# Kernel optimization log

Measured on AMD Instinct MI355X. Metric: run time of the kernel, lower is better.

The kernel has to match this reference:

```python
import jax, jax.numpy as jnp
import numpy as np

C = 256
C8 = C // 8
B, H, W = 4, 64, 64


def setup_inputs() -> dict:
    key = jax.random.key(0)
    ks = jax.random.split(key, 10)
    s = lambda fan_in: 1.0 / np.sqrt(fan_in)
    return {
        "x": jax.random.normal(ks[0], (B, C, H, W), dtype=jnp.float32),
        "conv_w": jax.random.normal(ks[1], (C8, C), dtype=jnp.float32) * s(C),
        "conv_b": jax.random.normal(ks[2], (C8,), dtype=jnp.float32) * 0.01,
        "q_w": jax.random.normal(ks[3], (C8, C8), dtype=jnp.float32) * s(C8),
        "q_b": jax.random.normal(ks[4], (C8,), dtype=jnp.float32) * 0.01,
        "k_w": jax.random.normal(ks[5], (C8, C8), dtype=jnp.float32) * s(C8),
        "k_b": jax.random.normal(ks[6], (C8,), dtype=jnp.float32) * 0.01,
        "v_w": jax.random.normal(ks[7], (C, C8), dtype=jnp.float32) * s(C8),
        "v_b": jax.random.normal(ks[8], (C,), dtype=jnp.float32) * 0.01,
        "gamma": jax.random.normal(ks[9], (1,), dtype=jnp.float32) * 0.1,
    }


def reference(x, conv_w, conv_b, q_w, q_b, k_w, k_b, v_w, v_b, gamma):
    b, c, h, w = x.shape
    hw = h * w
    # 1x1 convs are channel-mixing matmuls over flattened spatial dims
    xf = x.reshape(b, c, hw)                                   # [B, C, HW]
    proj = jnp.einsum('dc,bcn->bdn', conv_w, xf) + conv_b[None, :, None]   # [B, C8, HW]
    q = jnp.einsum('ed,bdn->bne', q_w, proj) + q_b[None, None, :]          # [B, HW, C8]
    k = jnp.einsum('ed,bdn->ben', k_w, proj) + k_b[None, :, None]          # [B, C8, HW]
    v = jnp.einsum('cd,bdn->bcn', v_w, proj) + v_b[None, :, None]          # [B, C, HW]
    attn = jax.nn.softmax(jnp.einsum('bne,bem->bnm', q, k), axis=-1)       # [B, HW, HW]
    out = jnp.einsum('bcm,bnm->bcn', v, attn)                              # [B, C, HW]
    out = out.reshape(b, c, h, w)
    return gamma[0] * out + x
```

## Files before the change

### kernel.cpp

```cpp
#include <hip/hip_runtime.h>
#include <hip/hip_bf16.h>
#include <stdint.h>

#define B_   4
#define C_   256
#define C8_  32
#define HW_  4096
#define ROWS_ 320
#define MS_  4
#define L2E  1.4426950408889634f

typedef __attribute__((ext_vector_type(8)))  short  short8;
typedef __attribute__((ext_vector_type(8)))  ushort us8;
typedef __attribute__((ext_vector_type(16))) float  f32x16;

#define WT_OFF    0
#define BALL_OFF  (256*320*4)
#define Q_OFF     (BALL_OFF + 1280)
#define KT_OFF    (Q_OFF  + B_*HW_*C8_*2)
#define V_OFF     (KT_OFF + B_*HW_*C8_*2)
#define PACC_OFF  (V_OFF  + B_*C_*HW_*2)
#define LPART_OFF (PACC_OFF + (size_t)MS_*B_*C_*HW_*2)

__device__ __forceinline__ ushort f2bf(float f) {
    union { float f; uint32_t u; } v; v.f = f;
    uint32_t u = v.u;
    uint32_t r = u + 0x7fffu + ((u >> 16) & 1u);
    return (ushort)(r >> 16);
}
__device__ __forceinline__ uint32_t pktr(float lo, float hi) {
    union { float f; uint32_t u; } a, b; a.f = lo; b.f = hi;
    return __builtin_amdgcn_perm(b.u, a.u, 0x07060302u);
}
__device__ __forceinline__ float fexp2(float s) {
    float y = fmaf(s, 8388608.0f, 1064992506.0f);
    y = fmaxf(y, 0.0f);
    union { int i; float f; } c; c.i = (int)y;
    return c.f;
}

__global__ __launch_bounds__(256) void k_setup(
    const float* __restrict__ conv_w, const float* __restrict__ conv_b,
    const float* __restrict__ q_w, const float* __restrict__ q_b,
    const float* __restrict__ k_w, const float* __restrict__ k_b,
    const float* __restrict__ v_w, const float* __restrict__ v_b,
    ushort* __restrict__ wbf, float* __restrict__ ball)
{
    int r = blockIdx.x;
    int c = threadIdx.x;
    const float* wrow;
    float bias;
    if (r < 32)       { wrow = q_w + r*32;      bias = q_b[r];      }
    else if (r < 64)  { wrow = k_w + (r-32)*32; bias = k_b[r-32];   }
    else              { wrow = v_w + (r-64)*32; bias = v_b[r-64];   }
    float acc = 0.f;
    #pragma unroll
    for (int d = 0; d < 32; ++d) acc += wrow[d] * conv_w[d*C_ + c];
    float scale = (r < 32) ? L2E : 1.0f;
    wbf[r*C_ + c] = f2bf(acc * scale);
    if (c == 0) {
        float bb = bias;
        #pragma unroll
        for (int d = 0; d < 32; ++d) bb += wrow[d] * conv_b[d];
        ball[r] = bb * scale;
    }
}

__global__ __launch_bounds__(320) void k_qkv(
    const float* __restrict__ x, const ushort* __restrict__ wbf,
    const float* __restrict__ ball,
    ushort* __restrict__ qg, ushort* __restrict__ ktg, ushort* __restrict__ vg)
{
    int blk = blockIdx.x;
    int b  = blk >> 7;
    int n0 = (blk & 127) * 32;
    int t = threadIdx.x;
    int w = t >> 6, lane = t & 63;
    int l31 = lane & 31, h = lane >> 5;

    f32x16 acc[2];
    acc[0] = (f32x16)(0.f);
    acc[1] = (f32x16)(0.f);

    const float* xb = x + (size_t)b*C_*HW_ + n0 + l31;
    const ushort* wr0 = wbf + (size_t)(w*64 + l31)*C_ + h*8;
    const ushort* wr1 = wr0 + 32*C_;

    #pragma unroll 2
    for (int kc = 0; kc < 16; ++kc) {
        int k0 = kc*16;
        short8 a0 = *(const short8*)(wr0 + k0);
        short8 a1 = *(const short8*)(wr1 + k0);
        const float* xc = xb + (size_t)(k0 + h*8)*HW_;
        union { uint32_t d[4]; short8 s8; } bf;
        #pragma unroll
        for (int j2 = 0; j2 < 4; ++j2) {
            float f0 = xc[(size_t)(2*j2    )*HW_];
            float f1 = xc[(size_t)(2*j2 + 1)*HW_];
            bf.d[j2] = pktr(f0, f1);
        }
        acc[0] = __builtin_amdgcn_mfma_f32_32x32x16_bf16(a0, bf.s8, acc[0], 0, 0, 0);
        acc[1] = __builtin_amdgcn_mfma_f32_32x32x16_bf16(a1, bf.s8, acc[1], 0, 0, 0);
    }

    int n = n0 + l31;
    #pragma unroll
    for (int mi = 0; mi < 2; ++mi) {
        int rowb = w*64 + mi*32;
        if (rowb == 0) {
            #pragma unroll
            for (int g = 0; g < 4; ++g) {
                int r0 = g*8 + 4*h;
                ushort4 pk;
                pk.x = f2bf(acc[mi][g*4+0] + ball[r0+0]);
                pk.y = f2bf(acc[mi][g*4+1] + ball[r0+1]);
                pk.z = f2bf(acc[mi][g*4+2] + ball[r0+2]);
                pk.w = f2bf(acc[mi][g*4+3] + ball[r0+3]);
                *(ushort4*)(qg + ((size_t)b*HW_ + n)*C8_ + r0) = pk;
            }
        } else if (rowb == 32) {
            #pragma unroll
            for (int g = 0; g < 4; ++g) {
                int e0 = g*8 + 4*h;
                ushort4 pk;
                pk.x = f2bf(acc[mi][g*4+0] + ball[32+e0+0]);
                pk.y = f2bf(acc[mi][g*4+1] + ball[32+e0+1]);
                pk.z = f2bf(acc[mi][g*4+2] + ball[32+e0+2]);
                pk.w = f2bf(acc[mi][g*4+3] + ball[32+e0+3]);
                *(ushort4*)(ktg + ((size_t)b*HW_ + n)*C8_ + e0) = pk;
            }
        } else {
            #pragma unroll
            for (int r = 0; r < 16; ++r) {
                int roff = (r & 3) + 8*(r >> 2) + 4*h;
                int c = rowb - 64 + roff;
                vg[((size_t)b*C_ + c)*HW_ + n] = f2bf(acc[mi][r] + ball[rowb + roff]);
            }
        }
    }
}

__global__ __launch_bounds__(256, 2) void k_attn(
    const ushort* __restrict__ qg, const ushort* __restrict__ ktg,
    const ushort* __restrict__ vg,
    ushort* __restrict__ pacc, float* __restrict__ lpart)
{
    __shared__ ushort v_lds[2][16*512];
    __shared__ ushort kt_lds[2][4*512];

    int blk = blockIdx.x;
    int ms = blk & 3;
    int cs = (blk >> 2) & 1;
    int qb = (blk >> 3) & 15;
    int b  = blk >> 7;
    int t = threadIdx.x;
    int w = t >> 6, lane = t & 63;
    int l31 = lane & 31, h = lane >> 5;
    int qbase = qb*256 + w*64;
    int mbase = ms*1024;

    const ushort* kb_p = ktg + (size_t)b*HW_*C8_;
    const ushort* vb_p = vg  + (size_t)b*C_*HW_ + (size_t)cs*128*HW_;

    short8 qf[2][2];
    #pragma unroll
    for (int qfr = 0; qfr < 2; ++qfr)
        #pragma unroll
        for (int ks = 0; ks < 2; ++ks)
            qf[qfr][ks] = *(const short8*)(qg + ((size_t)b*HW_ + qbase + qfr*32 + l31)*C8_
                                           + ks*16 + h*8);

    f32x16 acc[2][4];
    #pragma unroll
    for (int i = 0; i < 2; ++i)
        #pragma unroll
        for (int j = 0; j < 4; ++j)
            acc[i][j] = (f32x16)(0.f);
    float lsum[2] = {0.f, 0.f};

    #define STAGE(buf, m0)                                                          \
    {                                                                               \
        _Pragma("unroll")                                                           \
        for (int ks = 0; ks < 4; ++ks) {                                            \
            const ushort* src = vb_p + (size_t)(w*32 + l31)*HW_                     \
                                + (m0) + ks*16 + h*8;                               \
            __builtin_amdgcn_global_load_lds(                                       \
                (const __attribute__((address_space(1))) uint32_t*)src,             \
                (__attribute__((address_space(3))) uint32_t*)&v_lds[buf][(w*4+ks)*512], \
                16, 0, 0);                                                          \
        }                                                                           \
        {                                                                           \
            int kb = w >> 1, ks = w & 1;                                            \
            const ushort* src = kb_p + (size_t)((m0) + kb*32 + l31)*C8_             \
                                + ks*16 + h*8;                                      \
            __builtin_amdgcn_global_load_lds(                                       \
                (const __attribute__((address_space(1))) uint32_t*)src,             \
                (__attribute__((address_space(3))) uint32_t*)&kt_lds[buf][w*512],   \
                16, 0, 0);                                                          \
        }                                                                           \
    }

    STAGE(0, mbase)
    __syncthreads();

    int buf = 0;
    for (int it = 0; it < 16; ++it) {
        if (it + 1 < 16) STAGE(buf ^ 1, mbase + (it+1)*64)

        short8 ktf[2][2];
        #pragma unroll
        for (int kb = 0; kb < 2; ++kb)
            #pragma unroll
            for (int ks = 0; ks < 2; ++ks)
                ktf[kb][ks] = *(const short8*)(&kt_lds[buf][(kb*2+ks)*512 + lane*8]);

        uint32_t up[4][8];
        #pragma unroll
        for (int qfr = 0; qfr < 2; ++qfr) {
            #pragma unroll
            for (int kb = 0; kb < 2; ++kb) {
                f32x16 s = (f32x16)(0.f);
                s = __builtin_amdgcn_mfma_f32_32x32x16_bf16(ktf[kb][0], qf[qfr][0], s, 0, 0, 0);
                s = __builtin_amdgcn_mfma_f32_32x32x16_bf16(ktf[kb][1], qf[qfr][1], s, 0, 0, 0);
                float e[16];
                #pragma unroll
                for (int r = 0; r < 16; ++r) e[r] = fexp2(s[r]);
                float t0 = 0.f, t1 = 0.f;
                #pragma unroll
                for (int r = 0; r < 8; ++r) { t0 += e[2*r]; t1 += e[2*r+1]; }
                lsum[qfr] += t0 + t1;
                #pragma unroll
                for (int i = 0; i < 8; ++i)
                    up[qfr*2+kb][i] = pktr(e[2*i], e[2*i+1]);
            }
        }

        short8 pf[2][4];
        #pragma unroll
        for (int qfr = 0; qfr < 2; ++qfr) {
            #pragma unroll
            for (int kb = 0; kb < 2; ++kb) {
                uint32_t* u = up[qfr*2+kb];
                uint32_t bpA = (uint32_t)__shfl_xor((int)(h ? u[0] : u[2]), 32);
                uint32_t bpB = (uint32_t)__shfl_xor((int)(h ? u[1] : u[3]), 32);
                uint32_t bpC = (uint32_t)__shfl_xor((int)(h ? u[4] : u[6]), 32);
                uint32_t bpD = (uint32_t)__shfl_xor((int)(h ? u[5] : u[7]), 32);
                union { uint32_t d[4]; short8 s8; } fe, fo;
                fe.d[0] = h ? bpA : u[0];  fe.d[1] = h ? bpB : u[1];
                fe.d[2] = h ? u[2] : bpA;  fe.d[3] = h ? u[3] : bpB;
                fo.d[0] = h ? bpC : u[4];  fo.d[1] = h ? bpD : u[5];
                fo.d[2] = h ? u[6] : bpC;  fo.d[3] = h ? u[7] : bpD;
                pf[qfr][kb*2 + 0] = fe.s8;
                pf[qfr][kb*2 + 1] = fo.s8;
            }
        }

        #pragma unroll
        for (int ks = 0; ks < 4; ++ks) {
            #pragma unroll
            for (int cfr = 0; cfr < 4; ++cfr) {
                short8 vf = *(const short8*)(&v_lds[buf][(cfr*4+ks)*512 + lane*8]);
                acc[0][cfr] = __builtin_amdgcn_mfma_f32_32x32x16_bf16(vf, pf[0][ks], acc[0][cfr], 0, 0, 0);
                acc[1][cfr] = __builtin_amdgcn_mfma_f32_32x32x16_bf16(vf, pf[1][ks], acc[1][cfr], 0, 0, 0);
            }
        }
        __syncthreads();
        buf ^= 1;
    }

    #pragma unroll
    for (int qfr = 0; qfr < 2; ++qfr) {
        union { float f; int i; } cv; cv.f = lsum[qfr];
        cv.i = __shfl_xor(cv.i, 32);
        lsum[qfr] += cv.f;
    }
    if (cs == 0 && h == 0) {
        #pragma unroll
        for (int qfr = 0; qfr < 2; ++qfr)
            lpart[(size_t)(ms*B_ + b)*HW_ + qbase + qfr*32 + l31] = lsum[qfr];
    }

    int blkl = ((ms*B_ + b)*16 + qb)*2 + cs;
    #pragma unroll
    for (int qfr = 0; qfr < 2; ++qfr) {
        #pragma unroll
        for (int cfr = 0; cfr < 4; ++cfr) {
            union { uint32_t d[8]; us8 hlf[2]; } pk;
            #pragma unroll
            for (int i = 0; i < 8; ++i)
                pk.d[i] = pktr(acc[qfr][cfr][2*i], acc[qfr][cfr][2*i+1]);
            ushort* dst = pacc + ((size_t)(blkl*32 + (w*2 + qfr)*4 + cfr) << 10);
            *(us8*)(dst + lane*8)       = pk.hlf[0];
            *(us8*)(dst + 512 + lane*8) = pk.hlf[1];
        }
    }
    #undef STAGE
}

__global__ __launch_bounds__(256) void k_comb(
    const ushort* __restrict__ pacc, const float* __restrict__ lpart,
    const float* __restrict__ x, const float* __restrict__ gamma_p,
    float* __restrict__ out)
{
    int gid = blockIdx.x * 256 + threadIdx.x;
    int l31 = gid & 31;
    int h   = (gid >> 5) & 1;
    int cfr = (gid >> 6) & 3;
    int qfr = (gid >> 8) & 1;
    int w   = (gid >> 9) & 3;
    int cs  = (gid >> 11) & 1;
    int qb  = (gid >> 12) & 15;
    int b   = (gid >> 16) & 3;

    int q = qb*256 + w*64 + qfr*32 + l31;
    int frag = (w*2 + qfr)*4 + cfr;
    int lane = h*32 + l31;

    float sum[16];
    #pragma unroll
    for (int k = 0; k < 16; ++k) sum[k] = 0.f;
    float lt = 0.f;

    #pragma unroll
    for (int ms = 0; ms < MS_; ++ms) {
        int blkl = ((ms*B_ + b)*16 + qb)*2 + cs;
        const ushort* pp = pacc + ((size_t)(blkl*32 + frag) << 10) + lane*8;
        us8 a0 = *(const us8*)pp;
        us8 a1 = *(const us8*)(pp + 512);
        #pragma unroll
        for (int k = 0; k < 8; ++k) {
            union { uint32_t u; float f; } cv;
            cv.u = ((uint32_t)a0[k]) << 16;  sum[k]   += cv.f;
            cv.u = ((uint32_t)a1[k]) << 16;  sum[k+8] += cv.f;
        }
        lt += lpart[(size_t)(ms*B_ + b)*HW_ + q];
    }

    float g = gamma_p[0];
    float rl = g / lt;
    const float* xb = x + (size_t)b*C_*HW_ + q;
    float* ob = out + (size_t)b*C_*HW_ + q;
    #pragma unroll
    for (int k = 0; k < 16; ++k) {
        int c = cs*128 + cfr*32 + (k & 3) + 8*(k >> 2) + 4*h;
        size_t idx = (size_t)c*HW_;
        ob[idx] = sum[k]*rl + xb[idx];
    }
}

extern "C" void kernel_launch(void* const* d_in, const int* in_sizes, int n_in,
                              void* d_out, int out_size, void* d_ws, size_t ws_size,
                              hipStream_t stream)
{
    const float* x      = (const float*)d_in[0];
    const float* conv_w = (const float*)d_in[1];
    const float* conv_b = (const float*)d_in[2];
    const float* q_w    = (const float*)d_in[3];
    const float* q_b    = (const float*)d_in[4];
    const float* k_w    = (const float*)d_in[5];
    const float* k_b    = (const float*)d_in[6];
    const float* v_w    = (const float*)d_in[7];
    const float* v_b    = (const float*)d_in[8];
    const float* gamma  = (const float*)d_in[9];
    float* out = (float*)d_out;

    char* ws = (char*)d_ws;
    ushort* wbf   = (ushort*)(ws + WT_OFF);
    float*  ball  = (float*)(ws + BALL_OFF);
    ushort* qg    = (ushort*)(ws + Q_OFF);
    ushort* ktg   = (ushort*)(ws + KT_OFF);
    ushort* vg    = (ushort*)(ws + V_OFF);
    ushort* pacc  = (ushort*)(ws + PACC_OFF);
    float*  lpart = (float*)(ws + LPART_OFF);

    k_setup<<<ROWS_, 256, 0, stream>>>(conv_w, conv_b, q_w, q_b, k_w, k_b,
                                       v_w, v_b, wbf, ball);
    k_qkv<<<B_*128, 320, 0, stream>>>(x, wbf, ball, qg, ktg, vg);
    k_attn<<<512, 256, 0, stream>>>(qg, ktg, vg, pacc, lpart);
    k_comb<<<(B_*HW_*C_/16)/256, 256, 0, stream>>>(pacc, lpart, x, gamma, out);
}
```

Baseline: 179.0 us.

## Store Q/K/V and weights in MFMA fragment-native layout; double KV tile per stage

The setup and QKV kernels now write the fused weights, Q, K^T and V directly in a pre-swizzled fragment layout, with each 64-lane fragment contiguous in 512 elements. The attention kernel can then issue fully contiguous global-to-LDS loads and 16-byte per-lane reads instead of strided row gathers. The attention inner loop also stages 128 key positions per iteration instead of 64, which halves the number of barriers and pipeline steps. In exchange it doubles the LDS footprint, which may limit occupancy under launch_bounds(256,2). The V store in the QKV kernel is now scattered across fragment offsets.

```diff
diff --git a/kernel.cpp b/kernel.cpp
--- a/kernel.cpp
+++ b/kernel.cpp
@@ -57,7 +57,9 @@
     #pragma unroll
     for (int d = 0; d < 32; ++d) acc += wrow[d] * conv_w[d*C_ + c];
     float scale = (r < 32) ? L2E : 1.0f;
-    wbf[r*C_ + c] = f2bf(acc * scale);
+    int lanew = (r & 31) + 32*((c >> 3) & 1);
+    int fidx  = (c >> 4)*10 + (r >> 5);
+    wbf[fidx*512 + lanew*8 + (c & 7)] = f2bf(acc * scale);
     if (c == 0) {
         float bb = bias;
         #pragma unroll
@@ -83,14 +85,12 @@
     acc[1] = (f32x16)(0.f);
 
     const float* xb = x + (size_t)b*C_*HW_ + n0 + l31;
-    const ushort* wr0 = wbf + (size_t)(w*64 + l31)*C_ + h*8;
-    const ushort* wr1 = wr0 + 32*C_;
 
     #pragma unroll 2
     for (int kc = 0; kc < 16; ++kc) {
         int k0 = kc*16;
-        short8 a0 = *(const short8*)(wr0 + k0);
-        short8 a1 = *(const short8*)(wr1 + k0);
+        short8 a0 = *(const short8*)(wbf + (kc*10 + w*2    )*512 + lane*8);
+        short8 a1 = *(const short8*)(wbf + (kc*10 + w*2 + 1)*512 + lane*8);
         const float* xc = xb + (size_t)(k0 + h*8)*HW_;
         union { uint32_t d[4]; short8 s8; } bf;
         #pragma unroll
@@ -107,34 +107,35 @@
     #pragma unroll
     for (int mi = 0; mi < 2; ++mi) {
         int rowb = w*64 + mi*32;
-        if (rowb == 0) {
-            #pragma unroll
-            for (int g = 0; g < 4; ++g) {
-                int r0 = g*8 + 4*h;
-                ushort4 pk;
-                pk.x = f2bf(acc[mi][g*4+0] + ball[r0+0]);
-                pk.y = f2bf(acc[mi][g*4+1] + ball[r0+1]);
-                pk.z = f2bf(acc[mi][g*4+2] + ball[r0+2]);
-                pk.w = f2bf(acc[mi][g*4+3] + ball[r0+3]);
-                *(ushort4*)(qg + ((size_t)b*HW_ + n)*C8_ + r0) = pk;
-            }
-        } else if (rowb == 32) {
-            #pragma unroll
-            for (int g = 0; g < 4; ++g) {
-                int e0 = g*8 + 4*h;
-                ushort4 pk;
-                pk.x = f2bf(acc[mi][g*4+0] + ball[32+e0+0]);
-                pk.y = f2bf(acc[mi][g*4+1] + ball[32+e0+1]);
-                pk.z = f2bf(acc[mi][g*4+2] + ball[32+e0+2]);
-                pk.w = f2bf(acc[mi][g*4+3] + ball[32+e0+3]);
-                *(ushort4*)(ktg + ((size_t)b*HW_ + n)*C8_ + e0) = pk;
+        if (rowb < 64) {
+            ushort* dstb = (rowb == 0) ? qg : ktg;
+            int blkq = n0 >> 5;
+            #pragma unroll
+            for (int ks = 0; ks < 2; ++ks) {
+                #pragma unroll
+                for (int he = 0; he < 2; ++he) {
+                    int rb = ks*8 + he*4;
+                    int eb = rowb + ks*16 + he*8 + 4*h;
+                    ushort4 pk;
+                    pk.x = f2bf(acc[mi][rb+0] + ball[eb+0]);
+                    pk.y = f2bf(acc[mi][rb+1] + ball[eb+1]);
+                    pk.z = f2bf(acc[mi][rb+2] + ball[eb+2]);
+                    pk.w = f2bf(acc[mi][rb+3] + ball[eb+3]);
+                    size_t ad = ((size_t)((b*128 + blkq)*2 + ks)*64
+                                 + l31 + 32*he)*8 + 4*h;
+                    *(ushort4*)(dstb + ad) = pk;
+                }
             }
         } else {
+            int cblk = (rowb - 64) >> 5;
+            int mb = n >> 4;
+            int hn = (l31 >> 3) & 1;
+            int jj = l31 & 7;
+            size_t fb = ((size_t)(b*8 + cblk)*256 + mb)*512 + 32*hn*8 + jj;
             #pragma unroll
             for (int r = 0; r < 16; ++r) {
                 int roff = (r & 3) + 8*(r >> 2) + 4*h;
-                int c = rowb - 64 + roff;
-                vg[((size_t)b*C_ + c)*HW_ + n] = f2bf(acc[mi][r] + ball[rowb + roff]);
+                vg[fb + roff*8] = f2bf(acc[mi][r] + ball[rowb + roff]);
             }
         }
     }
@@ -145,8 +146,8 @@
     const ushort* __restrict__ vg,
     ushort* __restrict__ pacc, float* __restrict__ lpart)
 {
-    __shared__ ushort v_lds[2][16*512];
-    __shared__ ushort kt_lds[2][4*512];
+    __shared__ ushort v_lds[2][32*512];
+    __shared__ ushort kt_lds[2][8*512];
 
     int blk = blockIdx.x;
     int ms = blk & 3;
@@ -159,16 +160,13 @@
     int qbase = qb*256 + w*64;
     int mbase = ms*1024;
 
-    const ushort* kb_p = ktg + (size_t)b*HW_*C8_;
-    const ushort* vb_p = vg  + (size_t)b*C_*HW_ + (size_t)cs*128*HW_;
-
     short8 qf[2][2];
     #pragma unroll
     for (int qfr = 0; qfr < 2; ++qfr)
         #pragma unroll
         for (int ks = 0; ks < 2; ++ks)
-            qf[qfr][ks] = *(const short8*)(qg + ((size_t)b*HW_ + qbase + qfr*32 + l31)*C8_
-                                           + ks*16 + h*8);
+            qf[qfr][ks] = *(const short8*)(qg
+                + ((size_t)((b*128 + qb*8 + w*2 + qfr)*2 + ks)*64)*8 + lane*8);
 
     f32x16 acc[2][4];
     #pragma unroll
@@ -181,21 +179,21 @@
     #define STAGE(buf, m0)                                                          \
     {                                                                               \
         _Pragma("unroll")                                                           \
-        for (int ks = 0; ks < 4; ++ks) {                                            \
-            const ushort* src = vb_p + (size_t)(w*32 + l31)*HW_                     \
-                                + (m0) + ks*16 + h*8;                               \
+        for (int ms8 = 0; ms8 < 8; ++ms8) {                                         \
+            const ushort* src = vg + ((size_t)(b*8 + cs*4 + w)*256                  \
+                                 + ((m0) >> 4) + ms8)*512 + lane*8;                 \
             __builtin_amdgcn_global_load_lds(                                       \
                 (const __attribute__((address_space(1))) uint32_t*)src,             \
-                (__attribute__((address_space(3))) uint32_t*)&v_lds[buf][(w*4+ks)*512], \
+                (__attribute__((address_space(3))) uint32_t*)&v_lds[buf][(w*8+ms8)*512], \
                 16, 0, 0);                                                          \
         }                                                                           \
-        {                                                                           \
-            int kb = w >> 1, ks = w & 1;                                            \
-            const ushort* src = kb_p + (size_t)((m0) + kb*32 + l31)*C8_             \
-                                + ks*16 + h*8;                                      \
+        _Pragma("unroll")                                                           \
+        for (int ks = 0; ks < 2; ++ks) {                                            \
+            const ushort* src = ktg + ((size_t)((b*128 + ((m0) >> 5) + w)*2         \
+                                 + ks)*64)*8 + lane*8;                              \
             __builtin_amdgcn_global_load_lds(                                       \
                 (const __attribute__((address_space(1))) uint32_t*)src,             \
-                (__attribute__((address_space(3))) uint32_t*)&kt_lds[buf][w*512],   \
+                (__attribute__((address_space(3))) uint32_t*)&kt_lds[buf][(w*2+ks)*512], \
                 16, 0, 0);                                                          \
         }                                                                           \
     }
@@ -204,24 +202,20 @@
     __syncthreads();
 
     int buf = 0;
-    for (int it = 0; it < 16; ++it) {
-        if (it + 1 < 16) STAGE(buf ^ 1, mbase + (it+1)*64)
-
-        short8 ktf[2][2];
-        #pragma unroll
-        for (int kb = 0; kb < 2; ++kb)
-            #pragma unroll
-            for (int ks = 0; ks < 2; ++ks)
-                ktf[kb][ks] = *(const short8*)(&kt_lds[buf][(kb*2+ks)*512 + lane*8]);
-
-        uint32_t up[4][8];
-        #pragma unroll
-        for (int qfr = 0; qfr < 2; ++qfr) {
-            #pragma unroll
-            for (int kb = 0; kb < 2; ++kb) {
+    for (int it = 0; it < 8; ++it) {
+        if (it + 1 < 8) STAGE(buf ^ 1, mbase + (it+1)*128)
+
+        #pragma unroll
+        for (int kb = 0; kb < 4; ++kb) {
+            short8 kt0 = *(const short8*)(&kt_lds[buf][(kb*2+0)*512 + lane*8]);
+            short8 kt1 = *(const short8*)(&kt_lds[buf][(kb*2+1)*512 + lane*8]);
+
+            uint32_t up[2][8];
+            #pragma unroll
+            for (int qfr = 0; qfr < 2; ++qfr) {
                 f32x16 s = (f32x16)(0.f);
-                s = __builtin_amdgcn_mfma_f32_32x32x16_bf16(ktf[kb][0], qf[qfr][0], s, 0, 0, 0);
-                s = __builtin_amdgcn_mfma_f32_32x32x16_bf16(ktf[kb][1], qf[qfr][1], s, 0, 0, 0);
+                s = __builtin_amdgcn_mfma_f32_32x32x16_bf16(kt0, qf[qfr][0], s, 0, 0, 0);
+                s = __builtin_amdgcn_mfma_f32_32x32x16_bf16(kt1, qf[qfr][1], s, 0, 0, 0);
                 float e[16];
                 #pragma unroll
                 for (int r = 0; r < 16; ++r) e[r] = fexp2(s[r]);
@@ -230,17 +224,13 @@
                 for (int r = 0; r < 8; ++r) { t0 += e[2*r]; t1 += e[2*r+1]; }
                 lsum[qfr] += t0 + t1;
                 #pragma unroll
-                for (int i = 0; i < 8; ++i)
-                    up[qfr*2+kb][i] = pktr(e[2*i], e[2*i+1]);
-            }
-        }
-
-        short8 pf[2][4];
-        #pragma unroll
-        for (int qfr = 0; qfr < 2; ++qfr) {
-            #pragma unroll
-            for (int kb = 0; kb < 2; ++kb) {
-                uint32_t* u = up[qfr*2+kb];
+                for (int i = 0; i < 8; ++i) up[qfr][i] = pktr(e[2*i], e[2*i+1]);
+            }
+
+            short8 pf[2][2];
+            #pragma unroll
+            for (int qfr = 0; qfr < 2; ++qfr) {
+                uint32_t* u = up[qfr];
                 uint32_t bpA = (uint32_t)__shfl_xor((int)(h ? u[0] : u[2]), 32);
                 uint32_t bpB = (uint32_t)__shfl_xor((int)(h ? u[1] : u[3]), 32);
                 uint32_t bpC = (uint32_t)__shfl_xor((int)(h ? u[4] : u[6]), 32);
@@ -250,18 +240,19 @@
                 fe.d[2] = h ? u[2] : bpA;  fe.d[3] = h ? u[3] : bpB;
                 fo.d[0] = h ? bpC : u[4];  fo.d[1] = h ? bpD : u[5];
                 fo.d[2] = h ? u[6] : bpC;  fo.d[3] = h ? u[7] : bpD;
-                pf[qfr][kb*2 + 0] = fe.s8;
-                pf[qfr][kb*2 + 1] = fo.s8;
-            }
-        }
-
-        #pragma unroll
-        for (int ks = 0; ks < 4; ++ks) {
-            #pragma unroll
-            for (int cfr = 0; cfr < 4; ++cfr) {
-                short8 vf = *(const short8*)(&v_lds[buf][(cfr*4+ks)*512 + lane*8]);
-                acc[0][cfr] = __builtin_amdgcn_mfma_f32_32x32x16_bf16(vf, pf[0][ks], acc[0][cfr], 0, 0, 0);
-                acc[1][cfr] = __builtin_amdgcn_mfma_f32_32x32x16_bf16(vf, pf[1][ks], acc[1][cfr], 0, 0, 0);
+                pf[qfr][0] = fe.s8;
+                pf[qfr][1] = fo.s8;
+            }
+
+            #pragma unroll
+            for (int ksub = 0; ksub < 2; ++ksub) {
+                int ks16 = kb*2 + ksub;
+                #pragma unroll
+                for (int cfr = 0; cfr < 4; ++cfr) {
+                    short8 vf = *(const short8*)(&v_lds[buf][(cfr*8 + ks16)*512 + lane*8]);
+                    acc[0][cfr] = __builtin_amdgcn_mfma_f32_32x32x16_bf16(vf, pf[0][ksub], acc[0][cfr], 0, 0, 0);
+                    acc[1][cfr] = __builtin_amdgcn_mfma_f32_32x32x16_bf16(vf, pf[1][ksub], acc[1][cfr], 0, 0, 0);
+                }
             }
         }
         __syncthreads();
```

New measurement: 224.0 us. 25.1% more time.
